# Kernel tuning notes

Measured on AMD Instinct MI355X. Metric: run time of the kernel, lower is better.

The kernel has to match this reference:

```python
import jax, jax.numpy as jnp
import numpy as np
import math

E = 256; H = 8; MLP = 1024; LAT = 128; TOPK = 32
IH = 4; IDH = 8  # LightningIndexer: num_heads=4, indexer_head_dim=8
B, R, C = 2, 1024, 4


def setup_inputs() -> dict:
    key = jax.random.key(0)
    ks = jax.random.split(key, 12)
    s = 0.02
    def nrm(k, shape, scale=s):
        return jax.random.normal(k, shape, jnp.float32) * scale
    return {
        "src": jax.random.normal(ks[0], (B, R, C, E), jnp.float32),
        "train_test_split_index": 768,
        "fa_in_w": nrm(ks[1], (3 * E, E)), "fa_in_b": jnp.zeros((3 * E,), jnp.float32),
        "fa_out_w": nrm(ks[2], (E, E)), "fa_out_b": jnp.zeros((E,), jnp.float32),
        "norm1_g": jnp.ones((E,), jnp.float32), "norm1_b": jnp.zeros((E,), jnp.float32),
        "idx_q_w": nrm(ks[3], (IH * IDH, E)), "idx_k_w": nrm(ks[4], (IH * IDH, E)),
        "idx_out_w": jax.random.normal(ks[5], (IH,), jnp.float32),
        "mla_q_w": nrm(ks[6], (E, E)), "mla_down_w": nrm(ks[7], (LAT, E)),
        "mla_up_w": nrm(ks[8], (2 * E, LAT)), "mla_out_w": nrm(ks[9], (E, E)),
        "norm2_g": jnp.ones((E,), jnp.float32), "norm2_b": jnp.zeros((E,), jnp.float32),
        "lin1_w": nrm(ks[10], (MLP, E)), "lin1_b": jnp.zeros((MLP,), jnp.float32),
        "lin2_w": nrm(ks[11], (E, MLP)), "lin2_b": jnp.zeros((E,), jnp.float32),
        "norm3_g": jnp.ones((E,), jnp.float32), "norm3_b": jnp.zeros((E,), jnp.float32),
    }


def _ln(x, g, b, eps=1e-5):
    m = x.mean(-1, keepdims=True)
    v = ((x - m) ** 2).mean(-1, keepdims=True)
    return (x - m) * jax.lax.rsqrt(v + eps) * g + b


def _mha(x, in_w, in_b, out_w, out_b):
    # torch nn.MultiheadAttention, batch_first, self-attention
    Bf, S, D = x.shape
    dh = D // H
    qkv = x @ in_w.T + in_b
    q, k, v = jnp.split(qkv, 3, axis=-1)
    q = q.reshape(Bf, S, H, dh); k = k.reshape(Bf, S, H, dh); v = v.reshape(Bf, S, H, dh)
    a = jnp.einsum('bqhd,bkhd->bhqk', q, k) / math.sqrt(dh)
    a = jax.nn.softmax(a, axis=-1)
    o = jnp.einsum('bhqk,bkhd->bqhd', a, v).reshape(Bf, S, D)
    return o @ out_w.T + out_b


def _indexer(xq, xk, qw, kw, ow, top_k):
    # int8-quantized scoring: matmul -> scale -> relu -> head-weighted sum -> topk
    Bf, NQ, _ = xq.shape
    NK = xk.shape[1]
    q = (xq @ qw.T).reshape(Bf, NQ, IH, IDH).transpose(0, 2, 1, 3)  # [B,IH,NQ,IDH]
    k = (xk @ kw.T).reshape(Bf, NK, IH, IDH).transpose(0, 2, 1, 3)
    qs = (jnp.abs(q).max(axis=(2, 3), keepdims=True) + 1e-6) / 127.0
    ks_ = (jnp.abs(k).max(axis=(2, 3), keepdims=True) + 1e-6) / 127.0
    qi = jnp.clip(jnp.round(q / qs), -127, 127)
    ki = jnp.clip(jnp.round(k / ks_), -127, 127)
    scores = jax.nn.relu(jnp.einsum('bhqd,bhkd->bhqk', qi, ki) * (qs * ks_))
    red = jnp.einsum('bhqk,h->bqk', scores, ow)
    _, idx = jax.lax.top_k(red, top_k)
    return idx  # [B, NQ, top_k]


def _mla_sparse(xq, xkv, idx, qw, dw, uw, ow):
    # gather per-query top-k compressed latents, up-project, attend
    Bf, NQ, D = xq.shape
    dh = D // H
    K = idx.shape[2]
    q = (xq @ qw.T).reshape(Bf, NQ, H, dh)
    c = xkv @ dw.T                                    # [B, NKV, LAT]
    c_sel = c[jnp.arange(Bf)[:, None, None], idx]     # [B, NQ, K, LAT]
    kv = (c_sel @ uw.T).reshape(Bf, NQ, K, 2, H, dh)
    k, v = kv[..., 0, :, :], kv[..., 1, :, :]
    score = (q[:, :, None, :, :] * k).sum(-1) / math.sqrt(dh)  # [B,NQ,K,H]
    w = jax.nn.softmax(score, axis=2)
    out = (w[..., None] * v).sum(axis=2).reshape(Bf, NQ, D)
    return out @ ow.T


def reference(src, train_test_split_index, fa_in_w, fa_in_b, fa_out_w, fa_out_b,
              norm1_g, norm1_b, idx_q_w, idx_k_w, idx_out_w,
              mla_q_w, mla_down_w, mla_up_w, mla_out_w,
              norm2_g, norm2_b, lin1_w, lin1_b, lin2_w, lin2_b, norm3_g, norm3_b):
    Bz, Rz, Cz, D = src.shape
    split = int(train_test_split_index)
    # feature attention across columns
    sf = src.reshape(Bz * Rz, Cz, D)
    sf = _mha(sf, fa_in_w, fa_in_b, fa_out_w, fa_out_b) + sf
    src = _ln(sf.reshape(Bz, Rz, Cz, D), norm1_g, norm1_b)
    # row attention with DSA sparse top-k selection
    st = src.transpose(0, 2, 1, 3).reshape(Bz * Cz, Rz, D)
    x_tr, x_te = st[:, :split], st[:, split:]
    k_sel = min(TOPK, split)
    tr_idx = _indexer(x_tr, x_tr, idx_q_w, idx_k_w, idx_out_w, k_sel)
    tr_out = _mla_sparse(x_tr, x_tr, tr_idx, mla_q_w, mla_down_w, mla_up_w, mla_out_w)
    te_idx = _indexer(x_te, x_tr, idx_q_w, idx_k_w, idx_out_w, k_sel)
    te_out = _mla_sparse(x_te, x_tr, te_idx, mla_q_w, mla_down_w, mla_up_w, mla_out_w)
    st = st + jnp.concatenate([tr_out, te_out], axis=1)
    src = st.reshape(Bz, Cz, Rz, D).transpose(0, 2, 1, 3)
    src = _ln(src, norm2_g, norm2_b)
    h = jax.nn.gelu(src @ lin1_w.T + lin1_b, approximate=False)
    src = h @ lin2_w.T + lin2_b + src
    return _ln(src, norm3_g, norm3_b)
```

## Files before the change

### kernel.cpp

```cpp
#include <hip/hip_runtime.h>
#include <hip/hip_bf16.h>
#include <cmath>

#define E_ 256
#define H_ 8
#define DH 32
#define MLPD 1024
#define LATD 128
#define TOPK_ 32
#define BB 2
#define RR 1024
#define CC 4
#define NT 8192
#define BF 8
#define SPLIT 768

using bf16x8 = __attribute__((ext_vector_type(8))) short;
using f32x4v = __attribute__((ext_vector_type(4))) float;

__device__ __forceinline__ unsigned short f2b(float x) {
    __hip_bfloat16 h = __float2bfloat16(x);
    return *reinterpret_cast<unsigned short*>(&h);
}

struct ConvArgs {
    const float* s[10];
    unsigned short* d[10];
    int cum[10];
};
__global__ __launch_bounds__(256) void convert_f2b(ConvArgs a, int totq)
{
    int q = blockIdx.x * 256 + threadIdx.x;
    if (q >= totq) return;
    int seg = 0;
    while (q >= a.cum[seg]) seg++;
    int lq = q - (seg ? a.cum[seg - 1] : 0);
    float4 v = ((const float4*)a.s[seg])[lq];
    ushort4 o;
    o.x = f2b(v.x); o.y = f2b(v.y); o.z = f2b(v.z); o.w = f2b(v.w);
    ((ushort4*)a.d[seg])[lq] = o;
}

template<int TM, int TN, int BIAS, int GELU, int RES, int AMAP, int OMAP, int OUTBF>
__global__ __launch_bounds__(256) void gemm_mfma(
    const unsigned short* __restrict__ A, const unsigned short* __restrict__ W,
    const float* __restrict__ bias, const float* __restrict__ res,
    float* __restrict__ Cf, unsigned short* __restrict__ Ch,
    int M, int N, int K)
{
    __shared__ __align__(16) unsigned short As[TM * 40];
    __shared__ __align__(16) unsigned short Bs[TN * 40];
    const int tid = threadIdx.x;
    const int lane = tid & 63, wave = tid >> 6;
    const int wr = wave >> 1, wc = wave & 1;
    const int m0 = blockIdx.y * TM, n0 = blockIdx.x * TN;

    int ra, kqa;
    if constexpr (TM == 128) { ra = tid >> 1; kqa = (tid & 1) * 16; }
    else                     { ra = tid >> 2; kqa = (tid & 3) * 8; }
    int rb, kqb;
    if constexpr (TN == 128) { rb = tid >> 1; kqb = (tid & 1) * 16; }
    else                     { rb = tid >> 2; kqb = (tid & 3) * 8; }

    int am = m0 + ra;
    size_t arow = AMAP ? ((size_t)(am / SPLIT) * RR + (am % SPLIT)) : (size_t)am;
    const unsigned short* Ap = A + arow * (size_t)K + kqa;
    const unsigned short* Bp = W + (size_t)(n0 + rb) * K + kqb;

    constexpr int FM = TM / 32, FN = TN / 32;
    f32x4v acc[FM][FN];
#pragma unroll
    for (int i = 0; i < FM; i++)
#pragma unroll
        for (int j = 0; j < FN; j++) acc[i][j] = (f32x4v){0.f, 0.f, 0.f, 0.f};

    const int kof = (lane >> 4) * 8;
    int arow_lds[FM], brow_lds[FN];
#pragma unroll
    for (int f = 0; f < FM; f++)
        arow_lds[f] = (wr * (TM / 2) + f * 16 + (lane & 15)) * 40 + kof;
#pragma unroll
    for (int f = 0; f < FN; f++)
        brow_lds[f] = (wc * (TN / 2) + f * 16 + (lane & 15)) * 40 + kof;

    for (int k0 = 0; k0 < K; k0 += 32) {
        int4 va0, va1, vb0, vb1;
        va0 = *(const int4*)(Ap + k0);
        if constexpr (TM == 128) va1 = *(const int4*)(Ap + k0 + 8);
        vb0 = *(const int4*)(Bp + k0);
        if constexpr (TN == 128) vb1 = *(const int4*)(Bp + k0 + 8);
        __syncthreads();
        *(int4*)&As[ra * 40 + kqa] = va0;
        if constexpr (TM == 128) *(int4*)&As[ra * 40 + kqa + 8] = va1;
        *(int4*)&Bs[rb * 40 + kqb] = vb0;
        if constexpr (TN == 128) *(int4*)&Bs[rb * 40 + kqb + 8] = vb1;
        __syncthreads();
        bf16x8 af[FM], bfr[FN];
#pragma unroll
        for (int f = 0; f < FM; f++) af[f] = *(const bf16x8*)&As[arow_lds[f]];
#pragma unroll
        for (int f = 0; f < FN; f++) bfr[f] = *(const bf16x8*)&Bs[brow_lds[f]];
#pragma unroll
        for (int fm = 0; fm < FM; fm++)
#pragma unroll
            for (int fn = 0; fn < FN; fn++)
                acc[fm][fn] = __builtin_amdgcn_mfma_f32_16x16x32_bf16(
                    af[fm], bfr[fn], acc[fm][fn], 0, 0, 0);
    }

#pragma unroll
    for (int fm = 0; fm < FM; fm++) {
#pragma unroll
        for (int r = 0; r < 4; r++) {
            int row = m0 + wr * (TM / 2) + fm * 16 + ((lane >> 4) << 2) + r;
            size_t orow;
            if (OMAP) {
                int bc = row >> 10, rr = row & 1023;
                int b = bc >> 2, c = bc & 3;
                orow = ((size_t)(b * RR + rr)) * CC + c;
            } else orow = (size_t)row;
#pragma unroll
            for (int fn = 0; fn < FN; fn++) {
                int col = n0 + wc * (TN / 2) + fn * 16 + (lane & 15);
                float v = acc[fm][fn][r];
                if (BIAS) v += bias[col];
                if (GELU) v = 0.5f * v * (1.0f + erff(v * 0.70710678118654752f));
                if (RES)  v += res[(size_t)row * N + col];
                if (OUTBF) Ch[orow * (size_t)N + col] = f2b(v);
                else       Cf[orow * (size_t)N + col] = v;
            }
        }
    }
}

__global__ __launch_bounds__(256) void fa_attn(const float* __restrict__ qkv,
                                               unsigned short* __restrict__ outb)
{
    int seq = blockIdx.x, tid = threadIdx.x;
    __shared__ float sq[4][E_], sk[4][E_], sv[4][E_];
    __shared__ float ss[H_][4][4];
    __shared__ float sw[H_][4][4];
    const float4* base = (const float4*)(qkv + (size_t)seq * 3072);
#pragma unroll
    for (int p = 0; p < 3; p++) {
        int pos = tid + p * 256;
        float4 v = base[pos];
        int i = pos / 192, c4 = pos % 192;
        if (c4 < 64)       *(float4*)&sq[i][c4 * 4] = v;
        else if (c4 < 128) *(float4*)&sk[i][(c4 - 64) * 4] = v;
        else               *(float4*)&sv[i][(c4 - 128) * 4] = v;
    }
    __syncthreads();
    if (tid < 128) {
        int h = tid >> 4, i = (tid >> 2) & 3, j = tid & 3;
        float s = 0;
        for (int d = 0; d < DH; d++) s += sq[i][h * DH + d] * sk[j][h * DH + d];
        ss[h][i][j] = s * 0.17677669529663688f;
    }
    __syncthreads();
    if (tid < 32) {
        int h = tid >> 2, i = tid & 3;
        float m = ss[h][i][0];
        for (int j = 1; j < 4; j++) m = fmaxf(m, ss[h][i][j]);
        float e[4], sum = 0;
        for (int j = 0; j < 4; j++) { e[j] = expf(ss[h][i][j] - m); sum += e[j]; }
        float inv = 1.0f / sum;
        for (int j = 0; j < 4; j++) sw[h][i][j] = e[j] * inv;
    }
    __syncthreads();
    int e = tid, h = e >> 5;
    for (int i = 0; i < 4; i++) {
        float o = 0;
        for (int j = 0; j < 4; j++) o += sw[h][i][j] * sv[j][e];
        outb[((size_t)(seq * 4 + i)) * E_ + e] = f2b(o);
    }
}

template<int OMAP, int WB>
__global__ __launch_bounds__(256) void ln_k(const float* __restrict__ in,
                                            const float* __restrict__ g,
                                            const float* __restrict__ bta,
                                            float* __restrict__ out,
                                            unsigned short* __restrict__ outh)
{
    int row = blockIdx.x * 4 + (threadIdx.x >> 6);
    int t = threadIdx.x & 63;
    float4 v = ((const float4*)(in + (size_t)row * E_))[t];
    float s = v.x + v.y + v.z + v.w;
#pragma unroll
    for (int o = 32; o >= 1; o >>= 1) s += __shfl_xor(s, o);
    float mean = s * (1.0f / E_);
    float dx0 = v.x - mean, dx1 = v.y - mean, dx2 = v.z - mean, dx3 = v.w - mean;
    float q = dx0 * dx0 + dx1 * dx1 + dx2 * dx2 + dx3 * dx3;
#pragma unroll
    for (int o = 32; o >= 1; o >>= 1) q += __shfl_xor(q, o);
    float inv = rsqrtf(q * (1.0f / E_) + 1e-5f);
    size_t orow;
    if (OMAP == 1) {
        int b = row >> 12, r = (row >> 2) & 1023, c = row & 3;
        orow = ((size_t)(b * CC + c)) * RR + r;
    } else orow = (size_t)row;
    int c0 = t * 4;
    float4 o;
    o.x = dx0 * inv * g[c0 + 0] + bta[c0 + 0];
    o.y = dx1 * inv * g[c0 + 1] + bta[c0 + 1];
    o.z = dx2 * inv * g[c0 + 2] + bta[c0 + 2];
    o.w = dx3 * inv * g[c0 + 3] + bta[c0 + 3];
    ((float4*)(out + orow * E_))[t] = o;
    if (WB) {
        ushort4 oh; oh.x = f2b(o.x); oh.y = f2b(o.y); oh.z = f2b(o.z); oh.w = f2b(o.w);
        ((ushort4*)(outh + orow * E_))[t] = oh;
    }
}

__global__ __launch_bounds__(256) void idx_scales(const float* __restrict__ qk32,
                                                  float* __restrict__ scl)
{
    int id = blockIdx.x;
    int type = id / 32, bf = (id % 32) >> 2, h = id & 3;
    int cofs = (type == 2) ? 32 : 0;
    int r0 = (type == 1) ? SPLIT : 0;
    int r1 = (type == 1) ? RR : SPLIT;
    float m = 0;
    for (int r = r0 + (int)threadIdx.x; r < r1; r += 256) {
        const float* p = qk32 + ((size_t)(bf * RR + r)) * 64 + cofs + h * 8;
        for (int dd = 0; dd < 8; dd++) m = fmaxf(m, fabsf(p[dd]));
    }
#pragma unroll
    for (int o = 32; o >= 1; o >>= 1) m = fmaxf(m, __shfl_xor(m, o));
    __shared__ float red[4];
    if ((threadIdx.x & 63) == 0) red[threadIdx.x >> 6] = m;
    __syncthreads();
    if (threadIdx.x == 0) {
        m = fmaxf(fmaxf(red[0], red[1]), fmaxf(red[2], red[3]));
        scl[id] = (m + 1e-6f) / 127.0f;
    }
}

__global__ __launch_bounds__(256) void idx_quantk(const float* __restrict__ qk32,
                                                  const float* __restrict__ scl,
                                                  signed char* __restrict__ ki8)
{
    int gi = blockIdx.x * 256 + threadIdx.x;
    int bf = gi / (SPLIT * 32);
    int rem = gi % (SPLIT * 32);
    int r = rem >> 5, d = rem & 31, h = d >> 3;
    float ks = scl[64 + bf * 4 + h];
    float v = qk32[((size_t)(bf * RR + r)) * 64 + 32 + d];
    float qq = fminf(fmaxf(rintf(v / ks), -127.f), 127.f);
    ki8[gi] = (signed char)qq;
}

__global__ __launch_bounds__(256) void idx_score_topk(const float* __restrict__ qk32,
                                                      const signed char* __restrict__ ki8,
                                                      const float* __restrict__ scl,
                                                      const float* __restrict__ ow,
                                                      int* __restrict__ idx_out)
{
    int bid = blockIdx.x, tid = threadIdx.x;
    int bf = bid >> 10, qr = bid & 1023;
    int sel = (qr < SPLIT) ? 0 : 32;
    __shared__ float qi[32];
    __shared__ float fac[4];
    __shared__ unsigned keyhi[SPLIT];
    __shared__ __align__(16) unsigned long long cand[SPLIT];
    __shared__ int hist[256], hist2[256], Sarr[256];
    __shared__ int bsel1, bsel2, ccnt;

    hist[tid] = 0; hist2[tid] = 0;
    if (tid == 0) ccnt = 0;
    if (tid < 32) {
        int h = tid >> 3;
        float qs = scl[sel + bf * 4 + h];
        float v = qk32[(size_t)bid * 64 + tid];
        qi[tid] = fminf(fmaxf(rintf(v / qs), -127.f), 127.f);
    }
    if (tid < 4) {
        float qs = scl[sel + bf * 4 + tid];
        float ks = scl[64 + bf * 4 + tid];
        fac[tid] = __fmul_rn(qs, ks);
    }
    __syncthreads();
    float ow0 = ow[0], ow1 = ow[1], ow2 = ow[2], ow3 = ow[3];
    for (int k = tid; k < SPLIT; k += 256) {
        const int4* kp4 = (const int4*)(ki8 + ((size_t)(bf * SPLIT + k)) * 32);
        int4 w0 = kp4[0], w1 = kp4[1];
        int wd[8] = {w0.x, w0.y, w0.z, w0.w, w1.x, w1.y, w1.z, w1.w};
        float owv[4] = {ow0, ow1, ow2, ow3};
        float r = 0;
#pragma unroll
        for (int h = 0; h < 4; h++) {
            float dot = 0.f;
#pragma unroll
            for (int b = 0; b < 2; b++) {
                unsigned int w = (unsigned int)wd[h * 2 + b];
#pragma unroll
                for (int by = 0; by < 4; by++) {
                    float kv = (float)((signed char)(w >> (8 * by)));
                    dot = fmaf(qi[h * 8 + b * 4 + by], kv, dot);
                }
            }
            float sc = fmaxf(__fmul_rn(dot, fac[h]), 0.f);
            r = __fadd_rn(r, __fmul_rn(sc, owv[h]));
        }
        unsigned int bitsv = __float_as_uint(r);
        unsigned int mono = (bitsv & 0x80000000u) ? ~bitsv : (bitsv | 0x80000000u);
        if (mono == 0x7FFFFFFFu) mono = 0x80000000u;
        keyhi[k] = mono;
        atomicAdd(&hist[mono >> 24], 1);
    }
    __syncthreads();
    if (tid < 64) {
        int4 h4 = *(const int4*)&hist[tid * 4];
        int local = h4.x + h4.y + h4.z + h4.w;
        int s = local;
#pragma unroll
        for (int o = 1; o < 64; o <<= 1) {
            int x = __shfl_down(s, o);
            if (tid + o < 64) s += x;
        }
        int sufE = s - local;
        Sarr[tid * 4 + 0] = sufE + h4.y + h4.z + h4.w;
        Sarr[tid * 4 + 1] = sufE + h4.z + h4.w;
        Sarr[tid * 4 + 2] = sufE + h4.w;
        Sarr[tid * 4 + 3] = sufE;
    }
    __syncthreads();
    if (Sarr[tid] < TOPK_ && Sarr[tid] + hist[tid] >= TOPK_) bsel1 = tid;
    __syncthreads();
    const int b1 = bsel1;
    const int S1 = Sarr[b1];
    for (int k = tid; k < SPLIT; k += 256) {
        unsigned mono = keyhi[k];
        if ((int)(mono >> 24) == b1) atomicAdd(&hist2[(mono >> 16) & 255], 1);
    }
    __syncthreads();
    if (tid < 64) {
        int4 h4 = *(const int4*)&hist2[tid * 4];
        int local = h4.x + h4.y + h4.z + h4.w;
        int s = local;
#pragma unroll
        for (int o = 1; o < 64; o <<= 1) {
            int x = __shfl_down(s, o);
            if (tid + o < 64) s += x;
        }
        int sufE = s - local;
        Sarr[tid * 4 + 0] = sufE + h4.y + h4.z + h4.w;
        Sarr[tid * 4 + 1] = sufE + h4.z + h4.w;
        Sarr[tid * 4 + 2] = sufE + h4.w;
        Sarr[tid * 4 + 3] = sufE;
    }
    __syncthreads();
    if (S1 + Sarr[tid] < TOPK_ && S1 + Sarr[tid] + hist2[tid] >= TOPK_) bsel2 = tid;
    __syncthreads();
    const int b2 = bsel2;
    for (int k = tid; k < SPLIT; k += 256) {
        unsigned mono = keyhi[k];
        int hi = mono >> 24, mid = (mono >> 16) & 255;
        if (hi > b1 || (hi == b1 && mid >= b2)) {
            int s = atomicAdd(&ccnt, 1);
            cand[s] = ((unsigned long long)mono << 10) | (unsigned)(1023 - k);
        }
    }
    __syncthreads();
    const int n = ccnt;
    for (int ci = tid; ci < n; ci += 256) {
        unsigned long long mine = cand[ci];
        int r = 0;
        for (int j = 0; j < n; j++) r += (cand[j] > mine);
        if (r < TOPK_)
            idx_out[(size_t)bid * TOPK_ + r] = 1023 - (int)(mine & 1023ull);
    }
}

__global__ __launch_bounds__(256) void mla_g(const float* __restrict__ qb,
                                             const float* __restrict__ uw,
                                             float* __restrict__ G)
{
    int qt = blockIdx.x, h = blockIdx.y, tid = threadIdx.x;
    __shared__ float Qs[64][33];
    __shared__ float Us[32][132];
    {
        int r = tid >> 2, c0 = (tid & 3) * 8;
        const float* srcp = qb + ((size_t)(qt * 64 + r)) * E_ + h * DH + c0;
        float4 a = ((const float4*)srcp)[0];
        float4 b = ((const float4*)srcp)[1];
        Qs[r][c0 + 0] = a.x; Qs[r][c0 + 1] = a.y; Qs[r][c0 + 2] = a.z; Qs[r][c0 + 3] = a.w;
        Qs[r][c0 + 4] = b.x; Qs[r][c0 + 5] = b.y; Qs[r][c0 + 6] = b.z; Qs[r][c0 + 7] = b.w;
    }
    {
        int d = tid >> 3, l0 = (tid & 7) * 16;
        const float* srcp = uw + (size_t)(h * DH + d) * LATD + l0;
#pragma unroll
        for (int ii = 0; ii < 4; ii++) {
            float4 v = ((const float4*)srcp)[ii];
            *(float4*)&Us[d][l0 + ii * 4] = v;
        }
    }
    __syncthreads();
    int rg = tid >> 5, l = (tid & 31) * 4;
    float acc[8][4];
#pragma unroll
    for (int i = 0; i < 8; i++)
#pragma unroll
        for (int j = 0; j < 4; j++) acc[i][j] = 0.f;
    for (int d = 0; d < DH; d++) {
        float4 u = *(const float4*)&Us[d][l];
#pragma unroll
        for (int i = 0; i < 8; i++) {
            float qv = Qs[rg * 8 + i][d];
            acc[i][0] += qv * u.x; acc[i][1] += qv * u.y;
            acc[i][2] += qv * u.z; acc[i][3] += qv * u.w;
        }
    }
#pragma unroll
    for (int i = 0; i < 8; i++) {
        float4 o = {acc[i][0], acc[i][1], acc[i][2], acc[i][3]};
        *(float4*)(G + ((size_t)(qt * 64 + rg * 8 + i)) * 1024 + h * 128 + l) = o;
    }
}

__global__ __launch_bounds__(256) void mla_attn(const float* __restrict__ G,
                                                const float* __restrict__ cb,
                                                const int* __restrict__ idxb,
                                                float* __restrict__ Mo)
{
    int bid = blockIdx.x, tid = threadIdx.x;
    int bf = bid >> 10;
    __shared__ float cs[32][132];
    __shared__ float gs[8][132];
    __shared__ float swt[32][8];
    __shared__ int sidx[32];
    if (tid < 32) sidx[tid] = idxb[(size_t)bid * 32 + tid];
    {
        int flat = tid * 4, h = flat >> 7, l = flat & 127;
        float4 gv = *(const float4*)(G + (size_t)bid * 1024 + flat);
        *(float4*)&gs[h][l] = gv;
    }
    __syncthreads();
    {
        int j = tid >> 3, l0 = (tid & 7) * 16;
        const float* srcp = cb + ((size_t)(bf * SPLIT + sidx[j])) * LATD + l0;
#pragma unroll
        for (int ii = 0; ii < 4; ii++) {
            float4 vv = ((const float4*)srcp)[ii];
            *(float4*)&cs[j][l0 + ii * 4] = vv;
        }
    }
    __syncthreads();
    {
        int j = tid >> 3, h = tid & 7;
        float s = 0;
#pragma unroll
        for (int lb = 0; lb < 32; lb++) {
            float4 c4 = *(const float4*)&cs[j][lb * 4];
            float4 g4 = *(const float4*)&gs[h][lb * 4];
            s += c4.x * g4.x + c4.y * g4.y + c4.z * g4.z + c4.w * g4.w;
        }
        swt[j][h] = s * 0.17677669529663688f;
    }
    __syncthreads();
    if (tid < 8) {
        float m = swt[0][tid];
        for (int j = 1; j < 32; j++) m = fmaxf(m, swt[j][tid]);
        float sum = 0;
        for (int j = 0; j < 32; j++) { float e = expf(swt[j][tid] - m); swt[j][tid] = e; sum += e; }
        float inv = 1.0f / sum;
        for (int j = 0; j < 32; j++) swt[j][tid] *= inv;
    }
    __syncthreads();
    {
        int flat = tid * 4, h = flat >> 7, l = flat & 127;
        float4 acc = {0, 0, 0, 0};
        for (int j = 0; j < 32; j++) {
            float w = swt[j][h];
            float4 c4 = *(const float4*)&cs[j][l];
            acc.x += w * c4.x; acc.y += w * c4.y; acc.z += w * c4.z; acc.w += w * c4.w;
        }
        *(float4*)(Mo + (size_t)bid * 1024 + flat) = acc;
    }
}

__global__ __launch_bounds__(256) void mla_out(const float* __restrict__ Mo,
                                               const float* __restrict__ uw,
                                               unsigned short* __restrict__ ob)
{
    int qt = blockIdx.x, h = blockIdx.y, tid = threadIdx.x;
    __shared__ float Ms[64][132];
    __shared__ float Us[32][129];
    {
        int r = tid >> 2, l0 = (tid & 3) * 32;
        const float* srcp = Mo + ((size_t)(qt * 64 + r)) * 1024 + h * 128 + l0;
#pragma unroll
        for (int ii = 0; ii < 8; ii++) {
            float4 v = ((const float4*)srcp)[ii];
            *(float4*)&Ms[r][l0 + ii * 4] = v;
        }
    }
    {
        int d = tid >> 3, l0 = (tid & 7) * 16;
        const float* srcp = uw + (size_t)(256 + h * DH + d) * LATD + l0;
#pragma unroll
        for (int ii = 0; ii < 4; ii++) {
            float4 v = ((const float4*)srcp)[ii];
            Us[d][l0 + ii * 4 + 0] = v.x; Us[d][l0 + ii * 4 + 1] = v.y;
            Us[d][l0 + ii * 4 + 2] = v.z; Us[d][l0 + ii * 4 + 3] = v.w;
        }
    }
    __syncthreads();
    int d = tid & 31, rg = tid >> 5;
    float acc[8] = {0, 0, 0, 0, 0, 0, 0, 0};
    for (int l = 0; l < 128; l++) {
        float u = Us[d][l];
#pragma unroll
        for (int i = 0; i < 8; i++) acc[i] += Ms[rg * 8 + i][l] * u;
    }
#pragma unroll
    for (int i = 0; i < 8; i++)
        ob[((size_t)(qt * 64 + rg * 8 + i)) * E_ + h * DH + d] = f2b(acc[i]);
}

extern "C" void kernel_launch(void* const* d_in, const int* in_sizes, int n_in,
                              void* d_out, int out_size, void* d_ws, size_t ws_size,
                              hipStream_t stream)
{
    (void)in_sizes; (void)n_in; (void)out_size; (void)ws_size;
    const float* src      = (const float*)d_in[0];
    const float* fa_in_w  = (const float*)d_in[2];
    const float* fa_in_b  = (const float*)d_in[3];
    const float* fa_out_w = (const float*)d_in[4];
    const float* fa_out_b = (const float*)d_in[5];
    const float* n1g = (const float*)d_in[6];
    const float* n1b = (const float*)d_in[7];
    const float* iqw = (const float*)d_in[8];
    const float* ikw = (const float*)d_in[9];
    const float* iow = (const float*)d_in[10];
    const float* mqw = (const float*)d_in[11];
    const float* mdw = (const float*)d_in[12];
    const float* muw = (const float*)d_in[13];
    const float* mow = (const float*)d_in[14];
    const float* n2g = (const float*)d_in[15];
    const float* n2b = (const float*)d_in[16];
    const float* l1w = (const float*)d_in[17];
    const float* l1b = (const float*)d_in[18];
    const float* l2w = (const float*)d_in[19];
    const float* l2b = (const float*)d_in[20];
    const float* n3g = (const float*)d_in[21];
    const float* n3b = (const float*)d_in[22];

    float* ws = (float*)d_ws;
    size_t off = 0;
    auto alloc = [&](size_t n) { float* p = ws + off; off += (n + 3) & ~(size_t)3; return p; };

    float* bigA = alloc((size_t)NT * 1024);
    float* Mh   = alloc((size_t)NT * 1024);
    float* tbuf = alloc((size_t)NT * E_);
    float* stb  = alloc((size_t)NT * E_);
    float* cb   = alloc((size_t)BF * SPLIT * LATD);
    unsigned short* actBF1 = (unsigned short*)alloc((size_t)NT * E_ / 2);
    unsigned short* actBF2 = (unsigned short*)alloc((size_t)NT * E_ / 2);
    float* qk32 = alloc((size_t)NT * 64);
    float* scl = alloc(128);
    int*   idxb = (int*)alloc((size_t)NT * 32);
    signed char* ki8 = (signed char*)alloc((size_t)NT * 32 / 4);
    unsigned short* w16 = (unsigned short*)alloc(950272 / 2 + 8);
    unsigned short* wqk16 = (unsigned short*)alloc(16384 / 2 + 8);

    unsigned short* fa_in_w16  = w16;
    unsigned short* fa_out_w16 = fa_in_w16 + 196608;
    unsigned short* mqw16      = fa_out_w16 + 65536;
    unsigned short* mdw16      = mqw16 + 65536;
    unsigned short* mow16      = mdw16 + 32768;
    unsigned short* l1w16      = mow16 + 65536;
    unsigned short* l2w16      = l1w16 + 262144;

    float* qkv = bigA;
    float* G   = bigA;
    float* x2  = bigA;
    float* Mbuf = Mh;
    unsigned short* h116 = (unsigned short*)Mh;
    float* qb = tbuf;
    unsigned short* src16  = actBF1;
    unsigned short* abuf16 = actBF1;
    unsigned short* stb16  = actBF1;
    unsigned short* ob16   = actBF2;
    unsigned short* x216   = actBF2;

    ConvArgs ca;
    const float* segs[10] = {src, fa_in_w, fa_out_w, mqw, mdw, mow, l1w, l2w, iqw, ikw};
    unsigned short* segd[10] = {src16, fa_in_w16, fa_out_w16, mqw16, mdw16, mow16, l1w16, l2w16,
                                wqk16, wqk16 + 8192};
    int segn[10] = {NT * E_, 196608, 65536, 65536, 32768, 65536, 262144, 262144, 8192, 8192};
    int cum = 0;
    for (int i = 0; i < 10; i++) { ca.s[i] = segs[i]; ca.d[i] = segd[i]; cum += segn[i] / 4; ca.cum[i] = cum; }
    int totq = cum;
    convert_f2b<<<(totq + 255) / 256, 256, 0, stream>>>(ca, totq);

    dim3 blk(256);
    gemm_mfma<128,128,1,0,0,0,0,0><<<dim3(6,64), blk, 0, stream>>>(src16, fa_in_w16, fa_in_b, nullptr, qkv, nullptr, NT, 768, 256);
    fa_attn<<<2048, blk, 0, stream>>>(qkv, abuf16);
    gemm_mfma<128,64,1,0,1,0,0,0><<<dim3(4,64), blk, 0, stream>>>(abuf16, fa_out_w16, fa_out_b, src, tbuf, nullptr, NT, 256, 256);
    ln_k<1,1><<<NT/4, blk, 0, stream>>>(tbuf, n1g, n1b, stb, stb16);
    gemm_mfma<128,64,0,0,0,0,0,0><<<dim3(1,64), blk, 0, stream>>>(stb16, wqk16, nullptr, nullptr, qk32, nullptr, NT, 64, 256);
    idx_scales<<<96, blk, 0, stream>>>(qk32, scl);
    idx_quantk<<<(BF * SPLIT * 32) / 256, blk, 0, stream>>>(qk32, scl, ki8);
    idx_score_topk<<<NT, blk, 0, stream>>>(qk32, ki8, scl, iow, idxb);
    gemm_mfma<64,64,0,0,0,1,0,0><<<dim3(2,96), blk, 0, stream>>>(stb16, mdw16, nullptr, nullptr, cb, nullptr, BF * SPLIT, 128, 256);
    gemm_mfma<128,64,0,0,0,0,0,0><<<dim3(4,64), blk, 0, stream>>>(stb16, mqw16, nullptr, nullptr, qb, nullptr, NT, 256, 256);
    mla_g<<<dim3(128,8), blk, 0, stream>>>(qb, muw, G);
    mla_attn<<<NT, blk, 0, stream>>>(G, cb, idxb, Mbuf);
    mla_out<<<dim3(128,8), blk, 0, stream>>>(Mbuf, muw, ob16);
    gemm_mfma<128,64,0,0,1,0,1,0><<<dim3(4,64), blk, 0, stream>>>(ob16, mow16, nullptr, stb, tbuf, nullptr, NT, 256, 256);
    ln_k<0,1><<<NT/4, blk, 0, stream>>>(tbuf, n2g, n2b, x2, x216);
    gemm_mfma<128,128,1,1,0,0,0,1><<<dim3(8,64), blk, 0, stream>>>(x216, l1w16, l1b, nullptr, nullptr, h116, NT, MLPD, 256);
    gemm_mfma<128,64,1,0,1,0,0,0><<<dim3(4,64), blk, 0, stream>>>(h116, l2w16, l2b, x2, tbuf, nullptr, NT, 256, MLPD);
    ln_k<0,0><<<NT/4, blk, 0, stream>>>(tbuf, n3g, n3b, (float*)d_out, nullptr);
}
```

Baseline: 328.3 us.

## Rewrite sparse MLA attention with bf16 MFMA and bf16 intermediates

The per-query sparse MLA attention kernel is rewritten as a 64-thread wavefront that uses bf16 16x16x32 MFMA for both the score product and the weighted latent sum, with the softmax done through shuffles. The latent cache, the G projection and the attention output are now stored as bf16 instead of fp32, which halves their memory traffic. The cost is lower precision in the intermediate activations and softmax weights, plus a transposed LDS staging of the selected latent rows.

```diff
diff --git a/kernel.cpp b/kernel.cpp
--- a/kernel.cpp
+++ b/kernel.cpp
@@ -21,6 +21,9 @@
 __device__ __forceinline__ unsigned short f2b(float x) {
     __hip_bfloat16 h = __float2bfloat16(x);
     return *reinterpret_cast<unsigned short*>(&h);
+}
+__device__ __forceinline__ float b2f(unsigned short u) {
+    return __uint_as_float(((unsigned)u) << 16);
 }
 
 struct ConvArgs {
@@ -375,7 +378,7 @@
 
 __global__ __launch_bounds__(256) void mla_g(const float* __restrict__ qb,
                                              const float* __restrict__ uw,
-                                             float* __restrict__ G)
+                                             unsigned short* __restrict__ G16)
 {
     int qt = blockIdx.x, h = blockIdx.y, tid = threadIdx.x;
     __shared__ float Qs[64][33];
@@ -415,73 +418,85 @@
     }
 #pragma unroll
     for (int i = 0; i < 8; i++) {
-        float4 o = {acc[i][0], acc[i][1], acc[i][2], acc[i][3]};
-        *(float4*)(G + ((size_t)(qt * 64 + rg * 8 + i)) * 1024 + h * 128 + l) = o;
-    }
-}
-
-__global__ __launch_bounds__(256) void mla_attn(const float* __restrict__ G,
-                                                const float* __restrict__ cb,
-                                                const int* __restrict__ idxb,
-                                                float* __restrict__ Mo)
-{
-    int bid = blockIdx.x, tid = threadIdx.x;
-    int bf = bid >> 10;
-    __shared__ float cs[32][132];
-    __shared__ float gs[8][132];
-    __shared__ float swt[32][8];
+        ushort4 o;
+        o.x = f2b(acc[i][0]); o.y = f2b(acc[i][1]);
+        o.z = f2b(acc[i][2]); o.w = f2b(acc[i][3]);
+        *(ushort4*)(G16 + ((size_t)(qt * 64 + rg * 8 + i)) * 1024 + h * 128 + l) = o;
+    }
+}
+
+__global__ __launch_bounds__(64) void mla_attn(const unsigned short* __restrict__ G16,
+                                               const unsigned short* __restrict__ cb16,
+                                               const int* __restrict__ idxb,
+                                               unsigned short* __restrict__ Mo16)
+{
+    const int bid = blockIdx.x, l = threadIdx.x;
+    const int bf = bid >> 10;
+    __shared__ __align__(16) unsigned short ct[128][40];
+    __shared__ __align__(16) unsigned short wT[16][40];
     __shared__ int sidx[32];
-    if (tid < 32) sidx[tid] = idxb[(size_t)bid * 32 + tid];
+    if (l < 32) sidx[l] = idxb[(size_t)bid * 32 + l];
+
+    const int n16 = l & 15, g = l >> 4;
+
     {
-        int flat = tid * 4, h = flat >> 7, l = flat & 127;
-        float4 gv = *(const float4*)(G + (size_t)bid * 1024 + flat);
-        *(float4*)&gs[h][l] = gv;
-    }
-    __syncthreads();
-    {
-        int j = tid >> 3, l0 = (tid & 7) * 16;
-        const float* srcp = cb + ((size_t)(bf * SPLIT + sidx[j])) * LATD + l0;
-#pragma unroll
-        for (int ii = 0; ii < 4; ii++) {
-            float4 vv = ((const float4*)srcp)[ii];
-            *(float4*)&cs[j][l0 + ii * 4] = vv;
-        }
-    }
-    __syncthreads();
-    {
-        int j = tid >> 3, h = tid & 7;
-        float s = 0;
-#pragma unroll
-        for (int lb = 0; lb < 32; lb++) {
-            float4 c4 = *(const float4*)&cs[j][lb * 4];
-            float4 g4 = *(const float4*)&gs[h][lb * 4];
-            s += c4.x * g4.x + c4.y * g4.y + c4.z * g4.z + c4.w * g4.w;
-        }
-        swt[j][h] = s * 0.17677669529663688f;
-    }
-    __syncthreads();
-    if (tid < 8) {
-        float m = swt[0][tid];
-        for (int j = 1; j < 32; j++) m = fmaxf(m, swt[j][tid]);
-        float sum = 0;
-        for (int j = 0; j < 32; j++) { float e = expf(swt[j][tid] - m); swt[j][tid] = e; sum += e; }
-        float inv = 1.0f / sum;
-        for (int j = 0; j < 32; j++) swt[j][tid] *= inv;
-    }
-    __syncthreads();
-    {
-        int flat = tid * 4, h = flat >> 7, l = flat & 127;
-        float4 acc = {0, 0, 0, 0};
-        for (int j = 0; j < 32; j++) {
-            float w = swt[j][h];
-            float4 c4 = *(const float4*)&cs[j][l];
-            acc.x += w * c4.x; acc.y += w * c4.y; acc.z += w * c4.z; acc.w += w * c4.w;
-        }
-        *(float4*)(Mo + (size_t)bid * 1024 + flat) = acc;
-    }
-}
-
-__global__ __launch_bounds__(256) void mla_out(const float* __restrict__ Mo,
+        int j = l >> 1, c0 = (l & 1) * 64;
+        const unsigned short* crow = cb16 + ((size_t)(bf * SPLIT + sidx[j])) * 128 + c0;
+#pragma unroll
+        for (int e = 0; e < 8; e++) {
+            uint4 v = *(const uint4*)(crow + e * 8);
+            unsigned short tmp[8];
+            *(uint4*)tmp = v;
+#pragma unroll
+            for (int t = 0; t < 8; t++) ct[c0 + e * 8 + t][j] = tmp[t];
+        }
+    }
+
+    const unsigned short* Ab = G16 + (size_t)bid * 1024 + (size_t)(l & 7) * 128 + g * 8;
+    const int j0 = sidx[n16], j1 = sidx[16 + n16];
+    const unsigned short* B0 = cb16 + ((size_t)(bf * SPLIT + j0)) * 128 + g * 8;
+    const unsigned short* B1 = cb16 + ((size_t)(bf * SPLIT + j1)) * 128 + g * 8;
+    f32x4v s0 = {0.f, 0.f, 0.f, 0.f}, s1 = {0.f, 0.f, 0.f, 0.f};
+#pragma unroll
+    for (int c = 0; c < 4; c++) {
+        bf16x8 a  = *(const bf16x8*)(Ab + c * 32);
+        bf16x8 b0 = *(const bf16x8*)(B0 + c * 32);
+        bf16x8 b1 = *(const bf16x8*)(B1 + c * 32);
+        s0 = __builtin_amdgcn_mfma_f32_16x16x32_bf16(a, b0, s0, 0, 0, 0);
+        s1 = __builtin_amdgcn_mfma_f32_16x16x32_bf16(a, b1, s1, 0, 0, 0);
+    }
+
+    const float scale = 0.17677669529663688f;
+#pragma unroll
+    for (int r = 0; r < 4; r++) {
+        float a0 = s0[r] * scale, a1 = s1[r] * scale;
+        float mx = fmaxf(a0, a1);
+#pragma unroll
+        for (int o = 1; o < 16; o <<= 1) mx = fmaxf(mx, __shfl_xor(mx, o));
+        float e0 = expf(a0 - mx), e1 = expf(a1 - mx);
+        float sm = e0 + e1;
+#pragma unroll
+        for (int o = 1; o < 16; o <<= 1) sm += __shfl_xor(sm, o);
+        float inv = 1.0f / sm;
+        wT[g * 4 + r][n16]      = f2b(e0 * inv);
+        wT[g * 4 + r][16 + n16] = f2b(e1 * inv);
+    }
+
+    bf16x8 aw = *(const bf16x8*)&wT[n16][g * 8];
+#pragma unroll
+    for (int t = 0; t < 8; t++) {
+        bf16x8 bc = *(const bf16x8*)&ct[t * 16 + n16][g * 8];
+        f32x4v m = {0.f, 0.f, 0.f, 0.f};
+        m = __builtin_amdgcn_mfma_f32_16x16x32_bf16(aw, bc, m, 0, 0, 0);
+        if (g < 2) {
+#pragma unroll
+            for (int r = 0; r < 4; r++)
+                Mo16[(size_t)bid * 1024 + (size_t)(g * 4 + r) * 128 + t * 16 + n16] = f2b(m[r]);
+        }
+    }
+}
+
+__global__ __launch_bounds__(256) void mla_out(const unsigned short* __restrict__ Mo16,
                                                const float* __restrict__ uw,
                                                unsigned short* __restrict__ ob)
 {
@@ -490,11 +505,14 @@
     __shared__ float Us[32][129];
     {
         int r = tid >> 2, l0 = (tid & 3) * 32;
-        const float* srcp = Mo + ((size_t)(qt * 64 + r)) * 1024 + h * 128 + l0;
-#pragma unroll
-        for (int ii = 0; ii < 8; ii++) {
-            float4 v = ((const float4*)srcp)[ii];
-            *(float4*)&Ms[r][l0 + ii * 4] = v;
+        const unsigned short* srcp = Mo16 + ((size_t)(qt * 64 + r)) * 1024 + h * 128 + l0;
+#pragma unroll
+        for (int ii = 0; ii < 4; ii++) {
+            uint4 v = ((const uint4*)srcp)[ii];
+            unsigned short u[8];
+            *(uint4*)u = v;
+#pragma unroll
+            for (int t = 0; t < 8; t++) Ms[r][l0 + ii * 8 + t] = b2f(u[t]);
         }
     }
     {
@@ -510,10 +528,10 @@
     __syncthreads();
     int d = tid & 31, rg = tid >> 5;
     float acc[8] = {0, 0, 0, 0, 0, 0, 0, 0};
-    for (int l = 0; l < 128; l++) {
-        float u = Us[d][l];
-#pragma unroll
-        for (int i = 0; i < 8; i++) acc[i] += Ms[rg * 8 + i][l] * u;
+    for (int ll = 0; ll < 128; ll++) {
+        float u = Us[d][ll];
+#pragma unroll
+        for (int i = 0; i < 8; i++) acc[i] += Ms[rg * 8 + i][ll] * u;
     }
 #pragma unroll
     for (int i = 0; i < 8; i++)
@@ -556,7 +574,7 @@
     float* Mh   = alloc((size_t)NT * 1024);
     float* tbuf = alloc((size_t)NT * E_);
     float* stb  = alloc((size_t)NT * E_);
-    float* cb   = alloc((size_t)BF * SPLIT * LATD);
+    float* cbws = alloc((size_t)BF * SPLIT * LATD / 2 + 16);
     unsigned short* actBF1 = (unsigned short*)alloc((size_t)NT * E_ / 2);
     unsigned short* actBF2 = (unsigned short*)alloc((size_t)NT * E_ / 2);
     float* qk32 = alloc((size_t)NT * 64);
@@ -575,11 +593,12 @@
     unsigned short* l2w16      = l1w16 + 262144;
 
     float* qkv = bigA;
-    float* G   = bigA;
+    unsigned short* G16 = (unsigned short*)bigA;
     float* x2  = bigA;
-    float* Mbuf = Mh;
+    unsigned short* Mo16 = (unsigned short*)Mh;
     unsigned short* h116 = (unsigned short*)Mh;
     float* qb = tbuf;
+    unsigned short* cb16 = (unsigned short*)cbws;
     unsigned short* src16  = actBF1;
     unsigned short* abuf16 = actBF1;
     unsigned short* stb16  = actBF1;
@@ -605,11 +624,11 @@
     idx_scales<<<96, blk, 0, stream>>>(qk32, scl);
     idx_quantk<<<(BF * SPLIT * 32) / 256, blk, 0, stream>>>(qk32, scl, ki8);
     idx_score_topk<<<NT, blk, 0, stream>>>(qk32, ki8, scl, iow, idxb);
-    gemm_mfma<64,64,0,0,0,1,0,0><<<dim3(2,96), blk, 0, stream>>>(stb16, mdw16, nullptr, nullptr, cb, nullptr, BF * SPLIT, 128, 256);
+    gemm_mfma<64,64,0,0,0,1,0,1><<<dim3(2,96), blk, 0, stream>>>(stb16, mdw16, nullptr, nullptr, nullptr, cb16, BF * SPLIT, 128, 256);
     gemm_mfma<128,64,0,0,0,0,0,0><<<dim3(4,64), blk, 0, stream>>>(stb16, mqw16, nullptr, nullptr, qb, nullptr, NT, 256, 256);
-    mla_g<<<dim3(128,8), blk, 0, stream>>>(qb, muw, G);
-    mla_attn<<<NT, blk, 0, stream>>>(G, cb, idxb, Mbuf);
-    mla_out<<<dim3(128,8), blk, 0, stream>>>(Mbuf, muw, ob16);
+    mla_g<<<dim3(128,8), blk, 0, stream>>>(qb, muw, G16);
+    mla_attn<<<NT, dim3(64), 0, stream>>>(G16, cb16, idxb, Mo16);
+    mla_out<<<dim3(128,8), blk, 0, stream>>>(Mo16, muw, ob16);
     gemm_mfma<128,64,0,0,1,0,1,0><<<dim3(4,64), blk, 0, stream>>>(ob16, mow16, nullptr, stb, tbuf, nullptr, NT, 256, 256);
     ln_k<0,1><<<NT/4, blk, 0, stream>>>(tbuf, n2g, n2b, x2, x216);
     gemm_mfma<128,128,1,1,0,0,0,1><<<dim3(8,64), blk, 0, stream>>>(x216, l1w16, l1b, nullptr, nullptr, h116, NT, MLPD, 256);
```

Measured after the change: 309.6 us. 5.7% less time.
